# Performance work log

Hardware: AMD Instinct MI355X
Metric: run time of the kernel (lower is better)

## Reference

```python
import jax, jax.numpy as jnp
import numpy as np

NB, S, D, B, T, KMAX = 7, 16, 128, 32, 2048, 31
KS = [31, 21, 15, 11, 7, 5, 3]  # per-band conv kernel sizes


def _ln(x, g, b, eps=1e-5):
    m = x.mean(-1, keepdims=True)
    v = ((x - m) ** 2).mean(-1, keepdims=True)
    return (x - m) * jax.lax.rsqrt(v + eps) * g + b


def setup_inputs() -> dict:
    key = jax.random.key(0)
    ks = jax.random.split(key, 18)
    n = lambda k, shape, s=0.02: jax.random.normal(k, shape, jnp.float32) * s
    # conv kernels zero-padded to KMAX=31; symmetric padding keeps SAME-conv
    # equivalent to Conv1d(kernel=k, padding=k//2)
    mask = np.zeros((NB, KMAX, 1, 1), np.float32)
    for i, k in enumerate(KS):
        off = (KMAX - k) // 2
        mask[i, off:off + k] = 1.0
    inp = {
        'x': jax.random.normal(ks[0], (B, T, S), jnp.float32),
        'conv_w': n(ks[1], (NB, KMAX, S, D)) * jnp.asarray(mask),
        'conv_b': n(ks[2], (NB, D)),
        'dec_g': jnp.ones((NB, D), jnp.float32),
        'dec_b': jnp.zeros((NB, D), jnp.float32),
        'n2_g': jnp.ones((NB, D), jnp.float32),
        'n2_b': jnp.zeros((NB, D), jnp.float32),
        'ffn_w1': n(ks[3], (NB, D, 2 * D)),
        'ffn_b1': n(ks[4], (NB, 2 * D)),
        'ffn_w2': n(ks[5], (NB, 2 * D, D)),
        'ffn_b2': n(ks[6], (NB, D)),
        'proj_w': n(ks[7], (NB, D, 4 * S)),
        'proj_b': n(ks[8], (NB, 4 * S)),
        'mix_w1': n(ks[9], (NB * 4 * S, 8 * S)),
        'mix_b1': n(ks[10], (8 * S,)),
        'mix_w2': n(ks[11], (8 * S, S)),
        'mix_b2': n(ks[12], (S,)),
    }
    return inp


def reference(x, conv_w, conv_b, dec_g, dec_b, n2_g, n2_b,
              ffn_w1, ffn_b1, ffn_w2, ffn_b2,
              proj_w, proj_b, mix_w1, mix_b1, mix_w2, mix_b2):
    # Spectral decomposition: per-band 1D conv + LayerNorm. [nb, B, T, D]
    conv1 = lambda w: jax.lax.conv_general_dilated(
        x, w, (1,), 'SAME', dimension_numbers=('NWC', 'WIO', 'NWC'))
    h = jax.vmap(conv1)(conv_w) + conv_b[:, None, None, :]
    h = _ln(h, dec_g[:, None, None, :], dec_b[:, None, None, :])
    # Band processors (empty history => residual FFN branch)
    z = _ln(h, n2_g[:, None, None, :], n2_b[:, None, None, :])
    u = jax.nn.gelu(jnp.einsum('nbtd,nde->nbte', z, ffn_w1)
                    + ffn_b1[:, None, None, :], approximate=False)
    band_out = h + (jnp.einsum('nbte,ned->nbtd', u, ffn_w2)
                    + ffn_b2[:, None, None, :])
    # Reconstruction: per-band projection, concat, mix MLP
    p = jnp.einsum('nbtd,ndp->nbtp', band_out, proj_w) + proj_b[:, None, None, :]
    cat = jnp.transpose(p, (1, 2, 0, 3)).reshape(x.shape[0], x.shape[1], -1)
    m = jax.nn.gelu(cat @ mix_w1 + mix_b1, approximate=False)
    return m @ mix_w2 + mix_b2
```

## Files before the change

### kernel.cpp

```cpp
#include <hip/hip_runtime.h>
#include <stdint.h>

#define NB   7
#define SIN  16
#define DD   128
#define BB   32
#define TT   2048
#define TM   64
#define KMAX 31

#define XWS  40
#define HS   136
#define US   264

#define O_CWT 0
#define O_W1T 458752
#define O_W2T 688128
#define O_WCT 917504
#define O_M2T 1032192
#define O_B1A 1034240
#define W_TOTAL 1034368

typedef short v8s __attribute__((ext_vector_type(8)));
typedef float v4f __attribute__((ext_vector_type(4)));

__device__ __forceinline__ unsigned short f2b(float f) {
    unsigned u = __float_as_uint(f);
    u += 0x7fffu + ((u >> 16) & 1u);
    return (unsigned short)(u >> 16);
}
__device__ __forceinline__ float b2f(unsigned short h) {
    return __uint_as_float(((unsigned)h) << 16);
}
__device__ __forceinline__ float gelu_fast(float x) {
    return x / (1.f + __expf(-1.702f * x));
}
__device__ __forceinline__ float gelu_exact(float x) {
    return 0.5f * x * (1.f + erff(x * 0.70710678118654752f));
}

__global__ void prep_weights(const float* __restrict__ conv_w,
                             const float* __restrict__ ffn_w1,
                             const float* __restrict__ ffn_w2,
                             const float* __restrict__ proj_w,
                             const float* __restrict__ mix_w1,
                             const float* __restrict__ mix_w2,
                             const float* __restrict__ proj_b,
                             const float* __restrict__ mix_b1,
                             unsigned short* __restrict__ wsb) {
    for (int i = blockIdx.x * 256 + threadIdx.x; i < W_TOTAL; i += gridDim.x * 256) {
        float v;
        int o = i;
        if (o < O_W1T) {
            int n = o / (128 * 512); int r = o % (128 * 512);
            int d = r / 512; int kf = r % 512;
            int k = kf >> 4, s = kf & 15;
            v = (k < KMAX) ? conv_w[((n * KMAX + k) * SIN + s) * DD + d] : 0.f;
        } else if ((o -= O_W1T) < (O_W2T - O_W1T)) {
            int n = o / (256 * 128); int r = o % (256 * 128);
            int e = r / 128; int k = r % 128;
            v = ffn_w1[(n * 128 + k) * 256 + e];
        } else if ((o -= (O_W2T - O_W1T)) < (O_WCT - O_W2T)) {
            int n = o / (128 * 256); int r = o % (128 * 256);
            int d = r / 256; int e = r % 256;
            v = ffn_w2[(n * 256 + e) * 128 + d];
        } else if ((o -= (O_WCT - O_W2T)) < (O_M2T - O_WCT)) {
            int n = o / (128 * 128); int r = o % (128 * 128);
            int c = r / 128; int k = r % 128;
            const float4* pw4 = (const float4*)(proj_w + ((size_t)(n * 128 + k)) * 64);
            float s = 0.f;
            #pragma unroll 4
            for (int j4 = 0; j4 < 16; j4++) {
                float4 p4 = pw4[j4];
                int jb = n * 64 + j4 * 4;
                s += p4.x * mix_w1[(jb + 0) * 128 + c]
                   + p4.y * mix_w1[(jb + 1) * 128 + c]
                   + p4.z * mix_w1[(jb + 2) * 128 + c]
                   + p4.w * mix_w1[(jb + 3) * 128 + c];
            }
            v = s;
        } else if ((o -= (O_M2T - O_WCT)) < (O_B1A - O_M2T)) {
            int o16 = o / 128; int c = o % 128;
            v = mix_w2[c * 16 + o16];
        } else {
            o -= (O_B1A - O_M2T);
            float s = mix_b1[o];
            for (int kk = 0; kk < 448; kk++)
                s += proj_b[kk] * mix_w1[kk * 128 + o];
            v = s;
        }
        wsb[i] = f2b(v);
    }
}

__global__ __launch_bounds__(256, 2)
void fused_main(const float* __restrict__ x,
                const float* __restrict__ conv_b,
                const float* __restrict__ dec_g, const float* __restrict__ dec_b,
                const float* __restrict__ n2_g,  const float* __restrict__ n2_b,
                const float* __restrict__ ffn_b1, const float* __restrict__ ffn_b2,
                const unsigned short* __restrict__ wsb,
                float* __restrict__ out,
                const float* __restrict__ mix_b2) {
    __shared__ __align__(16) unsigned short xw[95 * XWS];
    __shared__ __align__(16) unsigned short hbuf[TM * HS];
    __shared__ __align__(16) unsigned short zbuf[TM * HS];
    __shared__ __align__(16) unsigned short ubuf[TM * US];

    const int tid  = threadIdx.x;
    const int lane = tid & 63;
    const int w    = tid >> 6;
    const int l16  = lane & 15;
    const int quad = lane >> 4;
    const int bb   = blockIdx.x >> 5;
    const int t0   = (blockIdx.x & 31) * TM;

    const unsigned short* cwT = wsb + O_CWT;
    const unsigned short* w1T = wsb + O_W1T;
    const unsigned short* w2T = wsb + O_W2T;
    const unsigned short* wcT = wsb + O_WCT;
    const unsigned short* m2T = wsb + O_M2T;

    for (int i = tid; i < 95 * SIN; i += 256) {
        int r = i >> 4, s = i & 15;
        int t = t0 + r - 15;
        float v = (t >= 0 && t < TT) ? x[((long)bb * TT + t) * SIN + s] : 0.f;
        xw[r * XWS + s] = f2b(v);
    }

    v4f macc[4][2];
    #pragma unroll
    for (int a = 0; a < 4; a++)
        #pragma unroll
        for (int c = 0; c < 2; c++)
            macc[a][c] = (v4f){0.f, 0.f, 0.f, 0.f};

    __syncthreads();

    static const int lo_tab[NB] = {0, 64, 128, 160, 192, 192, 224};
    static const int hi_tab[NB] = {512, 416, 384, 352, 320, 288, 288};

    for (int n = 0; n < NB; ++n) {
        {
            v4f acc[4][2];
            #pragma unroll
            for (int mt = 0; mt < 4; mt++)
                #pragma unroll
                for (int nt = 0; nt < 2; nt++) acc[mt][nt] = (v4f){0.f, 0.f, 0.f, 0.f};
            const int colb = w * 32;
            const int lo = lo_tab[n], hi = hi_tab[n];
            for (int kf = lo; kf < hi; kf += 32) {
                const int tap  = (kf >> 4) + (quad >> 1);
                const int scol = (quad & 1) * 8;
                v8s a[4], bf[2];
                #pragma unroll
                for (int mt = 0; mt < 4; mt++)
                    a[mt] = *reinterpret_cast<const v8s*>(&xw[(mt * 16 + l16 + tap) * XWS + scol]);
                #pragma unroll
                for (int nt = 0; nt < 2; nt++)
                    bf[nt] = *reinterpret_cast<const v8s*>(
                        &cwT[(size_t)(n * 128 + colb + nt * 16 + l16) * 512 + kf + quad * 8]);
                #pragma unroll
                for (int mt = 0; mt < 4; mt++)
                    #pragma unroll
                    for (int nt = 0; nt < 2; nt++)
                        acc[mt][nt] = __builtin_amdgcn_mfma_f32_16x16x32_bf16(a[mt], bf[nt], acc[mt][nt], 0, 0, 0);
            }
            #pragma unroll
            for (int nt = 0; nt < 2; nt++) {
                const int col = colb + nt * 16 + l16;
                const float bias = conv_b[n * 128 + col];
                #pragma unroll
                for (int mt = 0; mt < 4; mt++)
                    #pragma unroll
                    for (int r = 0; r < 4; r++)
                        hbuf[(mt * 16 + quad * 4 + r) * HS + col] = f2b(acc[mt][nt][r] + bias);
            }
        }
        __syncthreads();

        {
            const int row = tid >> 2, q = tid & 3;
            float v[32], s1 = 0.f, s2 = 0.f;
            #pragma unroll
            for (int c8 = 0; c8 < 4; c8++) {
                v8s t8 = *reinterpret_cast<const v8s*>(&hbuf[row * HS + q * 32 + c8 * 8]);
                #pragma unroll
                for (int j = 0; j < 8; j++) {
                    float f = b2f((unsigned short)t8[j]);
                    v[c8 * 8 + j] = f; s1 += f; s2 += f * f;
                }
            }
            s1 += __shfl_xor(s1, 1); s2 += __shfl_xor(s2, 1);
            s1 += __shfl_xor(s1, 2); s2 += __shfl_xor(s2, 2);
            const float m1 = s1 * (1.f / 128.f);
            const float rs = rsqrtf(s2 * (1.f / 128.f) - m1 * m1 + 1e-5f);
            const float4* dg4 = (const float4*)(dec_g + n * 128);
            const float4* db4 = (const float4*)(dec_b + n * 128);
            float hv[32], t1 = 0.f, t2 = 0.f;
            #pragma unroll
            for (int c4 = 0; c4 < 8; c4++) {
                float4 g4 = dg4[q * 8 + c4], b4 = db4[q * 8 + c4];
                float ga[4] = {g4.x, g4.y, g4.z, g4.w};
                float ba[4] = {b4.x, b4.y, b4.z, b4.w};
                #pragma unroll
                for (int j = 0; j < 4; j++) {
                    float h = (v[c4 * 4 + j] - m1) * rs * ga[j] + ba[j];
                    hv[c4 * 4 + j] = h; t1 += h; t2 += h * h;
                    hbuf[row * HS + q * 32 + c4 * 4 + j] = f2b(h);
                }
            }
            t1 += __shfl_xor(t1, 1); t2 += __shfl_xor(t2, 1);
            t1 += __shfl_xor(t1, 2); t2 += __shfl_xor(t2, 2);
            const float m2 = t1 * (1.f / 128.f);
            const float rs2 = rsqrtf(t2 * (1.f / 128.f) - m2 * m2 + 1e-5f);
            const float4* ng4 = (const float4*)(n2_g + n * 128);
            const float4* nb4 = (const float4*)(n2_b + n * 128);
            #pragma unroll
            for (int c4 = 0; c4 < 8; c4++) {
                float4 g4 = ng4[q * 8 + c4], b4 = nb4[q * 8 + c4];
                float ga[4] = {g4.x, g4.y, g4.z, g4.w};
                float ba[4] = {b4.x, b4.y, b4.z, b4.w};
                #pragma unroll
                for (int j = 0; j < 4; j++) {
                    float z = (hv[c4 * 4 + j] - m2) * rs2 * ga[j] + ba[j];
                    zbuf[row * HS + q * 32 + c4 * 4 + j] = f2b(z);
                }
            }
        }
        __syncthreads();

        {
            v4f acc[4][4];
            #pragma unroll
            for (int mt = 0; mt < 4; mt++)
                #pragma unroll
                for (int et = 0; et < 4; et++) acc[mt][et] = (v4f){0.f, 0.f, 0.f, 0.f};
            const int eb = w * 64;
            #pragma unroll
            for (int kb = 0; kb < 128; kb += 32) {
                v8s a[4], bf[4];
                #pragma unroll
                for (int mt = 0; mt < 4; mt++)
                    a[mt] = *reinterpret_cast<const v8s*>(&zbuf[(mt * 16 + l16) * HS + kb + quad * 8]);
                #pragma unroll
                for (int et = 0; et < 4; et++)
                    bf[et] = *reinterpret_cast<const v8s*>(
                        &w1T[(size_t)(n * 256 + eb + et * 16 + l16) * 128 + kb + quad * 8]);
                #pragma unroll
                for (int mt = 0; mt < 4; mt++)
                    #pragma unroll
                    for (int et = 0; et < 4; et++)
                        acc[mt][et] = __builtin_amdgcn_mfma_f32_16x16x32_bf16(a[mt], bf[et], acc[mt][et], 0, 0, 0);
            }
            #pragma unroll
            for (int et = 0; et < 4; et++) {
                const int e = eb + et * 16 + l16;
                const float bias = ffn_b1[n * 256 + e];
                #pragma unroll
                for (int mt = 0; mt < 4; mt++)
                    #pragma unroll
                    for (int r = 0; r < 4; r++)
                        ubuf[(mt * 16 + quad * 4 + r) * US + e] = f2b(gelu_fast(acc[mt][et][r] + bias));
            }
        }
        __syncthreads();

        {
            v4f acc[4][2];
            #pragma unroll
            for (int mt = 0; mt < 4; mt++)
                #pragma unroll
                for (int nt = 0; nt < 2; nt++) acc[mt][nt] = (v4f){0.f, 0.f, 0.f, 0.f};
            const int dbs = w * 32;
            #pragma unroll
            for (int kb = 0; kb < 256; kb += 32) {
                v8s a[4], bf[2];
                #pragma unroll
                for (int mt = 0; mt < 4; mt++)
                    a[mt] = *reinterpret_cast<const v8s*>(&ubuf[(mt * 16 + l16) * US + kb + quad * 8]);
                #pragma unroll
                for (int nt = 0; nt < 2; nt++)
                    bf[nt] = *reinterpret_cast<const v8s*>(
                        &w2T[(size_t)(n * 128 + dbs + nt * 16 + l16) * 256 + kb + quad * 8]);
                #pragma unroll
                for (int mt = 0; mt < 4; mt++)
                    #pragma unroll
                    for (int nt = 0; nt < 2; nt++)
                        acc[mt][nt] = __builtin_amdgcn_mfma_f32_16x16x32_bf16(a[mt], bf[nt], acc[mt][nt], 0, 0, 0);
            }
            #pragma unroll
            for (int nt = 0; nt < 2; nt++) {
                const int col = dbs + nt * 16 + l16;
                const float bias = ffn_b2[n * 128 + col];
                #pragma unroll
                for (int mt = 0; mt < 4; mt++)
                    #pragma unroll
                    for (int r = 0; r < 4; r++) {
                        const int row = mt * 16 + quad * 4 + r;
                        float bo = acc[mt][nt][r] + bias + b2f(hbuf[row * HS + col]);
                        zbuf[row * HS + col] = f2b(bo);
                    }
            }
        }
        __syncthreads();

        {
            #pragma unroll
            for (int kb = 0; kb < 128; kb += 32) {
                v8s a[4], bf[2];
                #pragma unroll
                for (int mt = 0; mt < 4; mt++)
                    a[mt] = *reinterpret_cast<const v8s*>(&zbuf[(mt * 16 + l16) * HS + kb + quad * 8]);
                #pragma unroll
                for (int nt = 0; nt < 2; nt++)
                    bf[nt] = *reinterpret_cast<const v8s*>(
                        &wcT[(size_t)(n * 128 + w * 32 + nt * 16 + l16) * 128 + kb + quad * 8]);
                #pragma unroll
                for (int mt = 0; mt < 4; mt++)
                    #pragma unroll
                    for (int nt = 0; nt < 2; nt++)
                        macc[mt][nt] = __builtin_amdgcn_mfma_f32_16x16x32_bf16(a[mt], bf[nt], macc[mt][nt], 0, 0, 0);
            }
        }
    }

    #pragma unroll
    for (int nt = 0; nt < 2; nt++) {
        const int col = w * 32 + nt * 16 + l16;
        const float bias = b2f(wsb[O_B1A + col]);
        #pragma unroll
        for (int mt = 0; mt < 4; mt++)
            #pragma unroll
            for (int r = 0; r < 4; r++)
                zbuf[(mt * 16 + quad * 4 + r) * HS + col] = f2b(gelu_exact(macc[mt][nt][r] + bias));
    }
    __syncthreads();

    {
        v4f acc = (v4f){0.f, 0.f, 0.f, 0.f};
        #pragma unroll
        for (int kb = 0; kb < 128; kb += 32) {
            v8s a  = *reinterpret_cast<const v8s*>(&zbuf[(w * 16 + l16) * HS + kb + quad * 8]);
            v8s bf = *reinterpret_cast<const v8s*>(&m2T[(size_t)l16 * 128 + kb + quad * 8]);
            acc = __builtin_amdgcn_mfma_f32_16x16x32_bf16(a, bf, acc, 0, 0, 0);
        }
        const float bias = mix_b2[l16];
        #pragma unroll
        for (int r = 0; r < 4; r++) {
            const int row = w * 16 + quad * 4 + r;
            out[((long)bb * TT + t0 + row) * SIN + l16] = acc[r] + bias;
        }
    }
}

extern "C" void kernel_launch(void* const* d_in, const int* in_sizes, int n_in,
                              void* d_out, int out_size, void* d_ws, size_t ws_size,
                              hipStream_t stream) {
    (void)in_sizes; (void)n_in; (void)out_size; (void)ws_size;
    const float* x      = (const float*)d_in[0];
    const float* conv_w = (const float*)d_in[1];
    const float* conv_b = (const float*)d_in[2];
    const float* dec_g  = (const float*)d_in[3];
    const float* dec_b  = (const float*)d_in[4];
    const float* n2_g   = (const float*)d_in[5];
    const float* n2_b   = (const float*)d_in[6];
    const float* ffn_w1 = (const float*)d_in[7];
    const float* ffn_b1 = (const float*)d_in[8];
    const float* ffn_w2 = (const float*)d_in[9];
    const float* ffn_b2 = (const float*)d_in[10];
    const float* proj_w = (const float*)d_in[11];
    const float* proj_b = (const float*)d_in[12];
    const float* mix_w1 = (const float*)d_in[13];
    const float* mix_b1 = (const float*)d_in[14];
    const float* mix_w2 = (const float*)d_in[15];
    const float* mix_b2 = (const float*)d_in[16];
    unsigned short* wsb = (unsigned short*)d_ws;
    float* out = (float*)d_out;

    hipLaunchKernelGGL(prep_weights, dim3(512), dim3(256), 0, stream,
                       conv_w, ffn_w1, ffn_w2, proj_w, mix_w1, mix_w2,
                       proj_b, mix_b1, wsb);
    hipLaunchKernelGGL(fused_main, dim3(BB * (TT / TM)), dim3(256), 0, stream,
                       x, conv_b, dec_g, dec_b, n2_g, n2_b, ffn_b1, ffn_b2,
                       wsb, out, mix_b2);
}
```

Before: 426.5 us.

## Fold FFN second matmul into mix projection weights algebraically

```diff
diff --git a/kernel.cpp b/kernel.cpp
--- a/kernel.cpp
+++ b/kernel.cpp
@@ -15,12 +15,19 @@
 
 #define O_CWT 0
 #define O_W1T 458752
-#define O_W2T 688128
+#define O_WFT 688128
 #define O_WCT 917504
 #define O_M2T 1032192
 #define O_B1A 1034240
 #define W_TOTAL 1034368
 
+#define NSEG_CW  444416
+#define NSEG_PAD 14336
+#define NSEG_W1  229376
+#define NSEG_WC  114688
+#define NSEG_M2  2048
+#define NSEG_WF  229376
+
 typedef short v8s __attribute__((ext_vector_type(8)));
 typedef float v4f __attribute__((ext_vector_type(4)));
 
@@ -41,55 +48,77 @@
 
 __global__ void prep_weights(const float* __restrict__ conv_w,
                              const float* __restrict__ ffn_w1,
-                             const float* __restrict__ ffn_w2,
                              const float* __restrict__ proj_w,
                              const float* __restrict__ mix_w1,
                              const float* __restrict__ mix_w2,
-                             const float* __restrict__ proj_b,
-                             const float* __restrict__ mix_b1,
                              unsigned short* __restrict__ wsb) {
-    for (int i = blockIdx.x * 256 + threadIdx.x; i < W_TOTAL; i += gridDim.x * 256) {
-        float v;
-        int o = i;
-        if (o < O_W1T) {
-            int n = o / (128 * 512); int r = o % (128 * 512);
-            int d = r / 512; int kf = r % 512;
-            int k = kf >> 4, s = kf & 15;
-            v = (k < KMAX) ? conv_w[((n * KMAX + k) * SIN + s) * DD + d] : 0.f;
-        } else if ((o -= O_W1T) < (O_W2T - O_W1T)) {
-            int n = o / (256 * 128); int r = o % (256 * 128);
-            int e = r / 128; int k = r % 128;
-            v = ffn_w1[(n * 128 + k) * 256 + e];
-        } else if ((o -= (O_W2T - O_W1T)) < (O_WCT - O_W2T)) {
-            int n = o / (128 * 256); int r = o % (128 * 256);
-            int d = r / 256; int e = r % 256;
-            v = ffn_w2[(n * 256 + e) * 128 + d];
-        } else if ((o -= (O_WCT - O_W2T)) < (O_M2T - O_WCT)) {
-            int n = o / (128 * 128); int r = o % (128 * 128);
-            int c = r / 128; int k = r % 128;
-            const float4* pw4 = (const float4*)(proj_w + ((size_t)(n * 128 + k)) * 64);
-            float s = 0.f;
-            #pragma unroll 4
-            for (int j4 = 0; j4 < 16; j4++) {
-                float4 p4 = pw4[j4];
-                int jb = n * 64 + j4 * 4;
-                s += p4.x * mix_w1[(jb + 0) * 128 + c]
-                   + p4.y * mix_w1[(jb + 1) * 128 + c]
-                   + p4.z * mix_w1[(jb + 2) * 128 + c]
-                   + p4.w * mix_w1[(jb + 3) * 128 + c];
-            }
-            v = s;
-        } else if ((o -= (O_M2T - O_WCT)) < (O_B1A - O_M2T)) {
-            int o16 = o / 128; int c = o % 128;
-            v = mix_w2[c * 16 + o16];
-        } else {
-            o -= (O_B1A - O_M2T);
-            float s = mix_b1[o];
-            for (int kk = 0; kk < 448; kk++)
-                s += proj_b[kk] * mix_w1[kk * 128 + o];
-            v = s;
-        }
-        wsb[i] = f2b(v);
+    const int i0 = blockIdx.x * 256 + threadIdx.x;
+    const int stride = gridDim.x * 256;
+
+    for (int o = i0; o < NSEG_CW; o += stride) {
+        int n = o / 63488; int r = o % 63488;
+        int k = r >> 11; int s = (r >> 7) & 15; int d = r & 127;
+        float v = conv_w[((n * 31 + k) * 16 + s) * 128 + d];
+        wsb[(size_t)(n * 128 + d) * 512 + k * 16 + s] = f2b(v);
+    }
+    for (int o = i0; o < NSEG_PAD; o += stride) {
+        int n = o >> 11; int d = (o >> 4) & 127; int s = o & 15;
+        wsb[(size_t)(n * 128 + d) * 512 + 496 + s] = 0;
+    }
+    for (int o = i0; o < NSEG_W1; o += stride) {
+        int n = o >> 15; int k = (o >> 8) & 127; int e = o & 255;
+        float v = ffn_w1[(n * 128 + k) * 256 + e];
+        wsb[O_W1T + (size_t)(n * 256 + e) * 128 + k] = f2b(v);
+    }
+    for (int o = i0; o < NSEG_WC; o += stride) {
+        int n = o >> 14; int k = (o >> 7) & 127; int c = o & 127;
+        const float* pw = proj_w + (size_t)(n * 128 + k) * 64;
+        const float* mw = mix_w1 + (size_t)(n * 64) * 128 + c;
+        float s = 0.f;
+        #pragma unroll 8
+        for (int j = 0; j < 64; j++)
+            s += pw[j] * mw[(size_t)j * 128];
+        wsb[O_WCT + (size_t)(n * 128 + c) * 128 + k] = f2b(s);
+    }
+    for (int o = i0; o < NSEG_M2; o += stride) {
+        int o16 = o >> 7; int c = o & 127;
+        wsb[O_M2T + o16 * 128 + c] = f2b(mix_w2[c * 16 + o16]);
+    }
+}
+
+__global__ void prep_wf(const float* __restrict__ ffn_w2,
+                        const float* __restrict__ ffn_b2,
+                        const float* __restrict__ proj_b,
+                        const float* __restrict__ mix_w1,
+                        const float* __restrict__ mix_b1,
+                        unsigned short* __restrict__ wsb) {
+    const int i0 = blockIdx.x * 256 + threadIdx.x;
+    const int stride = gridDim.x * 256;
+
+    for (int o = i0; o < NSEG_WF; o += stride) {
+        int n = o >> 15; int r = o & 32767;
+        int e = r >> 7; int c = r & 127;
+        const float* w2 = ffn_w2 + (size_t)(n * 256 + e) * 128;
+        const unsigned short* wc = wsb + O_WCT + (size_t)(n * 128 + c) * 128;
+        float s = 0.f;
+        #pragma unroll 8
+        for (int d = 0; d < 128; d++)
+            s += w2[d] * b2f(wc[d]);
+        wsb[O_WFT + (size_t)(n * 128 + c) * 256 + e] = f2b(s);
+    }
+    for (int o = i0; o < 128; o += stride) {
+        float s = mix_b1[o];
+        #pragma unroll 8
+        for (int kk = 0; kk < 448; kk++)
+            s += proj_b[kk] * mix_w1[kk * 128 + o];
+        for (int n = 0; n < NB; n++) {
+            const unsigned short* wc = wsb + O_WCT + (size_t)(n * 128 + o) * 128;
+            const float* fb = ffn_b2 + n * 128;
+            #pragma unroll 8
+            for (int d = 0; d < 128; d++)
+                s += fb[d] * b2f(wc[d]);
+        }
+        wsb[O_B1A + o] = f2b(s);
     }
 }
 
@@ -98,7 +127,7 @@
                 const float* __restrict__ conv_b,
                 const float* __restrict__ dec_g, const float* __restrict__ dec_b,
                 const float* __restrict__ n2_g,  const float* __restrict__ n2_b,
-                const float* __restrict__ ffn_b1, const float* __restrict__ ffn_b2,
+                const float* __restrict__ ffn_b1,
                 const unsigned short* __restrict__ wsb,
                 float* __restrict__ out,
                 const float* __restrict__ mix_b2) {
@@ -117,7 +146,7 @@
 
     const unsigned short* cwT = wsb + O_CWT;
     const unsigned short* w1T = wsb + O_W1T;
-    const unsigned short* w2T = wsb + O_W2T;
+    const unsigned short* wfT = wsb + O_WFT;
     const unsigned short* wcT = wsb + O_WCT;
     const unsigned short* m2T = wsb + O_M2T;
 
@@ -263,59 +292,36 @@
                     for (int r = 0; r < 4; r++)
                         ubuf[(mt * 16 + quad * 4 + r) * US + e] = f2b(gelu_fast(acc[mt][et][r] + bias));
             }
-        }
-        __syncthreads();
-
-        {
-            v4f acc[4][2];
-            #pragma unroll
-            for (int mt = 0; mt < 4; mt++)
-                #pragma unroll
-                for (int nt = 0; nt < 2; nt++) acc[mt][nt] = (v4f){0.f, 0.f, 0.f, 0.f};
-            const int dbs = w * 32;
-            #pragma unroll
-            for (int kb = 0; kb < 256; kb += 32) {
-                v8s a[4], bf[2];
-                #pragma unroll
-                for (int mt = 0; mt < 4; mt++)
-                    a[mt] = *reinterpret_cast<const v8s*>(&ubuf[(mt * 16 + l16) * US + kb + quad * 8]);
-                #pragma unroll
-                for (int nt = 0; nt < 2; nt++)
-                    bf[nt] = *reinterpret_cast<const v8s*>(
-                        &w2T[(size_t)(n * 128 + dbs + nt * 16 + l16) * 256 + kb + quad * 8]);
-                #pragma unroll
-                for (int mt = 0; mt < 4; mt++)
-                    #pragma unroll
-                    for (int nt = 0; nt < 2; nt++)
-                        acc[mt][nt] = __builtin_amdgcn_mfma_f32_16x16x32_bf16(a[mt], bf[nt], acc[mt][nt], 0, 0, 0);
-            }
-            #pragma unroll
-            for (int nt = 0; nt < 2; nt++) {
-                const int col = dbs + nt * 16 + l16;
-                const float bias = ffn_b2[n * 128 + col];
-                #pragma unroll
-                for (int mt = 0; mt < 4; mt++)
-                    #pragma unroll
-                    for (int r = 0; r < 4; r++) {
-                        const int row = mt * 16 + quad * 4 + r;
-                        float bo = acc[mt][nt][r] + bias + b2f(hbuf[row * HS + col]);
-                        zbuf[row * HS + col] = f2b(bo);
-                    }
-            }
-        }
-        __syncthreads();
-
-        {
             #pragma unroll
             for (int kb = 0; kb < 128; kb += 32) {
                 v8s a[4], bf[2];
                 #pragma unroll
                 for (int mt = 0; mt < 4; mt++)
-                    a[mt] = *reinterpret_cast<const v8s*>(&zbuf[(mt * 16 + l16) * HS + kb + quad * 8]);
+                    a[mt] = *reinterpret_cast<const v8s*>(&hbuf[(mt * 16 + l16) * HS + kb + quad * 8]);
                 #pragma unroll
                 for (int nt = 0; nt < 2; nt++)
                     bf[nt] = *reinterpret_cast<const v8s*>(
                         &wcT[(size_t)(n * 128 + w * 32 + nt * 16 + l16) * 128 + kb + quad * 8]);
+                #pragma unroll
+                for (int mt = 0; mt < 4; mt++)
+                    #pragma unroll
+                    for (int nt = 0; nt < 2; nt++)
+                        macc[mt][nt] = __builtin_amdgcn_mfma_f32_16x16x32_bf16(a[mt], bf[nt], macc[mt][nt], 0, 0, 0);
+            }
+        }
+        __syncthreads();
+
+        {
+            #pragma unroll
+            for (int kb = 0; kb < 256; kb += 32) {
+                v8s a[4], bf[2];
+                #pragma unroll
+                for (int mt = 0; mt < 4; mt++)
+                    a[mt] = *reinterpret_cast<const v8s*>(&ubuf[(mt * 16 + l16) * US + kb + quad * 8]);
+                #pragma unroll
+                for (int nt = 0; nt < 2; nt++)
+                    bf[nt] = *reinterpret_cast<const v8s*>(
+                        &wfT[(size_t)(n * 128 + w * 32 + nt * 16 + l16) * 256 + kb + quad * 8]);
                 #pragma unroll
                 for (int mt = 0; mt < 4; mt++)
                     #pragma unroll
@@ -379,9 +385,10 @@
     float* out = (float*)d_out;
 
     hipLaunchKernelGGL(prep_weights, dim3(512), dim3(256), 0, stream,
-                       conv_w, ffn_w1, ffn_w2, proj_w, mix_w1, mix_w2,
-                       proj_b, mix_b1, wsb);
+                       conv_w, ffn_w1, proj_w, mix_w1, mix_w2, wsb);
+    hipLaunchKernelGGL(prep_wf, dim3(512), dim3(256), 0, stream,
+                       ffn_w2, ffn_b2, proj_b, mix_w1, mix_b1, wsb);
     hipLaunchKernelGGL(fused_main, dim3(BB * (TT / TM)), dim3(256), 0, stream,
-                       x, conv_b, dec_g, dec_b, n2_g, n2_b, ffn_b1, ffn_b2,
+                       x, conv_b, dec_g, dec_b, n2_g, n2_b, ffn_b1,
                        wsb, out, mix_b2);
 }
```

After: 447.9 us. +5.0%, slower.
